# Kernel optimization log

Measured on AMD Instinct MI355X. Metric: run time of the kernel, lower is better.

## Reference

```python
import jax, jax.numpy as jnp
import numpy as np

B, N, CS, CV, K = 8, 2048, 256, 128, 3
EPS = 1e-6


def _eq_layernorm(s, v):
    # scalars: standard layernorm over channels; vectors: RMS of channel norms (equivariant)
    mu = s.mean(-1, keepdims=True)
    var = ((s - mu) ** 2).mean(-1, keepdims=True)
    s = (s - mu) * jax.lax.rsqrt(var + EPS)
    n2 = (v ** 2).sum(-1).mean(-1, keepdims=True)  # [b,n,1]
    v = v * jax.lax.rsqrt(n2 + EPS)[..., None]
    return s, v


def setup_inputs() -> dict:
    key = jax.random.key(0)
    ks = jax.random.split(key, 7)
    fan_s = K * (CS + CV)       # 1152
    fan_v = K * (CS + 2 * CV)   # 1536
    return {
        "x_s": jax.random.normal(ks[0], (B, N, CS), jnp.float32),
        "x_v": jax.random.normal(ks[1], (B, N, CV, 3), jnp.float32),
        "coords": jax.random.normal(ks[2], (B, N, 3), jnp.float32) * 10.0,
        "W_conv_s": jax.random.normal(ks[3], (fan_s, CS), jnp.float32),
        "W_conv_v": jax.random.normal(ks[4], (fan_v, CV), jnp.float32),
        "W_si_s": jax.random.normal(ks[5], (CS, CS), jnp.float32),
        "W_si_v": jax.random.normal(ks[6], (CV, CV), jnp.float32),
    }


def reference(x_s, x_v, coords, W_conv_s, W_conv_v, W_si_s, W_si_v):
    b, n, cs = x_s.shape
    cv = x_v.shape[2]
    pad = K // 2
    # 'same' padding: zeros for features, edge for coords (zero displacement at boundary)
    sp = jnp.pad(x_s, ((0, 0), (pad, pad), (0, 0)))
    vp = jnp.pad(x_v, ((0, 0), (pad, pad), (0, 0), (0, 0)))
    cp = jnp.pad(coords, ((0, 0), (pad, pad), (0, 0)), mode="edge")
    s_win = jnp.stack([sp[:, k:k + n] for k in range(K)], 2)   # [b,n,K,cs]
    v_win = jnp.stack([vp[:, k:k + n] for k in range(K)], 2)   # [b,n,K,cv,3]
    c_win = jnp.stack([cp[:, k:k + n] for k in range(K)], 2)   # [b,n,K,3]

    d = c_win - coords[:, :, None, :]
    dn = jnp.linalg.norm(d, axis=-1, keepdims=True)
    rhat = d * jnp.where(dn > 1e-6, 1.0 / jnp.maximum(dn, 1e-6), 0.0)

    # Clebsch-Gordan paths of (0e,1e) features with sh = (1, rhat)
    vdot = jnp.einsum("bnkcd,bnkd->bnkc", v_win, rhat)                    # 1x1 -> 0
    scal_in = jnp.concatenate([s_win, vdot], -1).reshape(b, n, -1)        # [b,n,K*(cs+cv)]
    s_rhat = s_win[..., None] * rhat[:, :, :, None, :]                    # 0x1 -> 1
    v_cross = jnp.cross(v_win, rhat[:, :, :, None, :])                    # 1x1 -> 1
    vec_in = jnp.concatenate([v_win, s_rhat, v_cross], 3).reshape(b, n, -1, 3)

    # SequenceConvolution linear mixing (fan-in normalized) + norm=True
    h_s = jnp.einsum("bnp,po->bno", scal_in, W_conv_s) / float(np.sqrt(scal_in.shape[-1]))
    h_v = jnp.einsum("bnpd,po->bnod", vec_in, W_conv_v) / float(np.sqrt(vec_in.shape[2]))
    h_s, h_v = _eq_layernorm(h_s, h_v)

    # SelfInteraction: per-degree channel mixing, residual=True, norm_last=True
    y_s = h_s + h_s @ W_si_s / float(np.sqrt(cs))
    y_v = h_v + jnp.einsum("bncd,co->bnod", h_v, W_si_v) / float(np.sqrt(cv))
    y_s, y_v = _eq_layernorm(y_s, y_v)

    # block Residual + final EquivariantLayerNorm
    z_s, z_v = _eq_layernorm(x_s + y_s, x_v + y_v)
    return z_s, z_v
```

## Files before the change

kernel.cpp:

```cpp
#include <hip/hip_runtime.h>
#include <hip/hip_bf16.h>


typedef __attribute__((ext_vector_type(8))) short short8;
typedef __attribute__((ext_vector_type(4))) float f32x4;
typedef unsigned short u16;

#define B_   8
#define N_   2048
#define EPS_ 1e-6f
#define TB   64

#define OFF_CS 0
#define OFF_V  294912
#define OFF_G  393216
#define OFF_SS 491520
#define OFF_SV 557056

#define MFMA(a,b,c) __builtin_amdgcn_mfma_f32_16x16x32_bf16((a),(b),(c),0,0,0)

__device__ __forceinline__ u16 f2b(float v){ __hip_bfloat16 h=__float2bfloat16(v); return *(u16*)&h; }

__global__ __launch_bounds__(256) void prep_weights(
    const float* __restrict__ Wcs, const float* __restrict__ Wcv,
    const float* __restrict__ Wss, const float* __restrict__ Wsv,
    u16* __restrict__ ws)
{
    const int bid = blockIdx.x;
    const float* src; int N, r0, ld, c0; u16* dst; int tile;
    if (bid < 288)      { src=Wcs; N=256; r0=0; dst=ws+OFF_CS; ld=1152; c0=0; tile=bid; }
    else if (bid < 336) { int k=(bid-288)/16; tile=(bid-288)%16;
                          src=Wcv; N=128; r0=k*512;     dst=ws+OFF_V; ld=768; c0=k*256; }
    else if (bid < 432) { int k=(bid-336)/32; tile=(bid-336)%32;
                          src=Wcv; N=128; r0=k*512+128; dst=ws+OFF_G; ld=768; c0=k*256; }
    else if (bid < 480) { int k=(bid-432)/16; tile=(bid-432)%16;
                          src=Wcv; N=128; r0=k*512+384; dst=ws+OFF_V; ld=768; c0=k*256+128; }
    else if (bid < 544) { tile=bid-480; src=Wss; N=256; r0=0; dst=ws+OFF_SS; ld=256; c0=0; }
    else                { tile=bid-544; src=Wsv; N=128; r0=0; dst=ws+OFF_SV; ld=128; c0=0; }
    const int ntN = N >> 5;
    const int kt = (tile/ntN)*32, nn = (tile%ntN)*32;
    __shared__ float t[32][33];
    const int r = threadIdx.x >> 5, c = threadIdx.x & 31;
#pragma unroll
    for (int i = 0; i < 4; ++i)
        t[r+8*i][c] = src[(size_t)(r0+kt+r+8*i)*N + nn+c];
    __syncthreads();
#pragma unroll
    for (int i = 0; i < 4; ++i)
        dst[(size_t)(nn+r+8*i)*ld + c0+kt+c] = f2b(t[c][r+8*i]);
}

__device__ __forceinline__ void ln_reduce(
    float p1[4][4], float p2[4][4], float pv[4][4], f32x4* red,
    int tid, int lm, int lq4, int w,
    float mu[4][4], float ss[4][4], float vs[4][4])
{
    __syncthreads();
#pragma unroll
    for (int m2 = 1; m2 < 16; m2 <<= 1)
#pragma unroll
        for (int m = 0; m < 4; ++m)
#pragma unroll
            for (int q = 0; q < 4; ++q) {
                p1[m][q] += __shfl_xor(p1[m][q], m2);
                p2[m][q] += __shfl_xor(p2[m][q], m2);
                pv[m][q] += __shfl_xor(pv[m][q], m2);
            }
    if (lm == 0)
#pragma unroll
        for (int m = 0; m < 4; ++m)
#pragma unroll
            for (int q = 0; q < 4; ++q) {
                f32x4 r = {p1[m][q], p2[m][q], pv[m][q], 0.f};
                red[(m*16+lq4+q)*8 + w] = r;
            }
    __syncthreads();
    if (tid < 64) {
        const int t = tid;
        f32x4 rs = red[t*8+0];
#pragma unroll
        for (int i = 1; i < 8; ++i) rs += red[t*8+i];
        const float mm = rs.x * (1.f/256.f);
        f32x4 fin;
        fin.x = mm;
        fin.y = rsqrtf(rs.y*(1.f/256.f) - mm*mm + EPS_);
        fin.z = rsqrtf(rs.z*(1.f/128.f) + EPS_);
        fin.w = 0.f;
        red[t*8 + (t&7)] = fin;
    }
    __syncthreads();
#pragma unroll
    for (int m = 0; m < 4; ++m)
#pragma unroll
        for (int q = 0; q < 4; ++q) {
            const int t = m*16 + lq4 + q;
            const f32x4 fin = red[t*8 + (t&7)];
            mu[m][q] = fin.x; ss[m][q] = fin.y; vs[m][q] = fin.z;
        }
}

__global__ __launch_bounds__(512, 2) void mixing_main(
    const float* __restrict__ x_s, const float* __restrict__ x_v,
    const float* __restrict__ coords, const u16* __restrict__ wt,
    float* __restrict__ out)
{
    __shared__ __align__(16) char smem[162816];
    u16*   fs  = (u16*)smem;
    u16*   fv  = (u16*)(smem + 50176);
    u16*   hsb = (u16*)smem;
    u16*   hvb = (u16*)(smem + 50176);
    float* xvL = (float*)(smem + 50176);
    float* rhp = (float*)(smem + 151552);
    f32x4* red = (f32x4*)(smem + 154624);

    const int tid = threadIdx.x;
    const int w   = tid >> 6, l = tid & 63;
    const int lm  = l & 15, lk8 = (l >> 4) << 3, lq4 = (l >> 4) << 2;
    const int wh2 = w & 3;
    const int th  = w >> 2;
    const int gt0 = blockIdx.x * TB;
    const int n0  = gt0 & (N_ - 1);
    const int seq0 = gt0 - n0;
    const size_t ZV0 = (size_t)B_ * N_ * 256;

    if (tid < 192) {
        const int t = tid / 3, k = tid - 3 * (tid / 3);
        const int jn = n0 + t + k - 1;
        const int jc = jn < 0 ? 0 : (jn > N_-1 ? N_-1 : jn);
        const float* cj = coords + (size_t)(seq0 + jc) * 3;
        const float* c0p = coords + (size_t)(gt0 + t) * 3;
        const float d0 = cj[0]-c0p[0], d1 = cj[1]-c0p[1], d2 = cj[2]-c0p[2];
        const float dn = sqrtf(d0*d0 + d1*d1 + d2*d2);
        const float inv = dn > 1e-6f ? 1.f/dn : 0.f;
        rhp[(t*3+k)*4+0] = d0*inv; rhp[(t*3+k)*4+1] = d1*inv; rhp[(t*3+k)*4+2] = d2*inv;
    }
    __syncthreads();

    const f32x4 fz = {0.f,0.f,0.f,0.f};
    f32x4 acc_s[4][2];
    f32x4 accv[3][2][2];
#pragma unroll
    for (int m = 0; m < 4; ++m) { acc_s[m][0] = fz; acc_s[m][1] = fz; }
#pragma unroll
    for (int d = 0; d < 3; ++d)
#pragma unroll
        for (int tf = 0; tf < 2; ++tf) { accv[d][tf][0] = fz; accv[d][tf][1] = fz; }

    const int bt = tid >> 3;
    const int bx = tid & 7;

#pragma unroll 1
    for (int k = 0; k < 3; ++k) {
        const int jn = n0 + bt + k - 1;
        const bool valid = (unsigned)jn < (unsigned)N_;
        const size_t j = (size_t)seq0 + (valid ? jn : 0);
        {
            const int c0 = bx * 32;
            const float4* sp = (const float4*)(x_s + j*256 + c0);
#pragma unroll
            for (int h = 0; h < 4; ++h) {
                float v[8];
                if (valid) {
                    const float4 f0 = sp[2*h], f1 = sp[2*h+1];
                    v[0]=f0.x; v[1]=f0.y; v[2]=f0.z; v[3]=f0.w;
                    v[4]=f1.x; v[5]=f1.y; v[6]=f1.z; v[7]=f1.w;
                } else {
#pragma unroll
                    for (int i = 0; i < 8; ++i) v[i] = 0.f;
                }
                short8 p;
#pragma unroll
                for (int i = 0; i < 8; ++i) p[i] = (short)f2b(v[i]);
                *(short8*)(fs + bt*392 + c0 + 8*h) = p;
            }
        }
        {
            const int ch0 = bx * 16;
            const float r0 = rhp[(bt*3+k)*4+0];
            const float r1 = rhp[(bt*3+k)*4+1];
            const float r2 = rhp[(bt*3+k)*4+2];
#pragma unroll
            for (int hh = 0; hh < 2; ++hh) {
                const int cb = ch0 + 8*hh;
                float vv[24];
                if (valid) {
                    const float4* vp = (const float4*)(x_v + ((size_t)j*128 + cb)*3);
#pragma unroll
                    for (int i = 0; i < 6; ++i) {
                        const float4 f = vp[i];
                        vv[4*i]=f.x; vv[4*i+1]=f.y; vv[4*i+2]=f.z; vv[4*i+3]=f.w;
                    }
                } else {
#pragma unroll
                    for (int i = 0; i < 24; ++i) vv[i] = 0.f;
                }
                short8 dv, w0, w1, w2, x0, x1, x2;
#pragma unroll
                for (int m = 0; m < 8; ++m) {
                    const float a0 = vv[3*m], a1 = vv[3*m+1], a2 = vv[3*m+2];
                    dv[m] = (short)f2b(a0*r0 + a1*r1 + a2*r2);
                    w0[m] = (short)f2b(a0); w1[m] = (short)f2b(a1); w2[m] = (short)f2b(a2);
                    x0[m] = (short)f2b(a1*r2 - a2*r1);
                    x1[m] = (short)f2b(a2*r0 - a0*r2);
                    x2[m] = (short)f2b(a0*r1 - a1*r0);
                }
                *(short8*)(fs + bt*392 + 256 + cb)            = dv;
                *(short8*)(fv + (0*64+bt)*264 + cb)           = w0;
                *(short8*)(fv + (1*64+bt)*264 + cb)           = w1;
                *(short8*)(fv + (2*64+bt)*264 + cb)           = w2;
                *(short8*)(fv + (0*64+bt)*264 + 128 + cb)     = x0;
                *(short8*)(fv + (1*64+bt)*264 + 128 + cb)     = x1;
                *(short8*)(fv + (2*64+bt)*264 + 128 + cb)     = x2;
            }
        }

        const u16* bS0 = wt + OFF_CS + k*384 + (size_t)((2*w+0)*16+lm)*1152;
        const u16* bS1 = wt + OFF_CS + k*384 + (size_t)((2*w+1)*16+lm)*1152;
        const u16* bG0 = wt + OFF_G  + k*256 + (size_t)((2*wh2+0)*16+lm)*768;
        const u16* bG1 = wt + OFF_G  + k*256 + (size_t)((2*wh2+1)*16+lm)*768;
        const u16* bV0 = wt + OFF_V  + k*256 + (size_t)((2*wh2+0)*16+lm)*768;
        const u16* bV1 = wt + OFF_V  + k*256 + (size_t)((2*wh2+1)*16+lm)*768;
        short8 Bs0[3], Bs1[3];
#pragma unroll
        for (int i = 0; i < 3; ++i) {
            Bs0[i] = *(const short8*)(bS0 + i*32 + lk8);
            Bs1[i] = *(const short8*)(bS1 + i*32 + lk8);
        }
        short8 pg0 = *(const short8*)(bG0 + lk8);
        short8 pg1 = *(const short8*)(bG1 + lk8);
        short8 pv0 = *(const short8*)(bV0 + lk8);
        short8 pv1 = *(const short8*)(bV1 + lk8);
        __syncthreads();

        f32x4 agc[2][2] = {{fz,fz},{fz,fz}};
#pragma unroll
        for (int ks = 0; ks < 12; ++ks) {
            const int r = ks % 3;
            const short8 b0 = Bs0[r], b1 = Bs1[r];
            if (ks + 3 < 12) {
                Bs0[r] = *(const short8*)(bS0 + (ks+3)*32 + lk8);
                Bs1[r] = *(const short8*)(bS1 + (ks+3)*32 + lk8);
            }
            const int ko = ks*32 + lk8;
            const short8 a0 = *(const short8*)(fs + ( 0+lm)*392 + ko);
            const short8 a1 = *(const short8*)(fs + (16+lm)*392 + ko);
            const short8 a2 = *(const short8*)(fs + (32+lm)*392 + ko);
            const short8 a3 = *(const short8*)(fs + (48+lm)*392 + ko);
            acc_s[0][0] = MFMA(a0, b0, acc_s[0][0]);
            acc_s[0][1] = MFMA(a0, b1, acc_s[0][1]);
            acc_s[1][0] = MFMA(a1, b0, acc_s[1][0]);
            acc_s[1][1] = MFMA(a1, b1, acc_s[1][1]);
            acc_s[2][0] = MFMA(a2, b0, acc_s[2][0]);
            acc_s[2][1] = MFMA(a2, b1, acc_s[2][1]);
            acc_s[3][0] = MFMA(a3, b0, acc_s[3][0]);
            acc_s[3][1] = MFMA(a3, b1, acc_s[3][1]);
            if (ks < 8) {
                const short8 g0 = pg0, g1 = pg1;
                if (ks < 7) {
                    pg0 = *(const short8*)(bG0 + (ks+1)*32 + lk8);
                    pg1 = *(const short8*)(bG1 + (ks+1)*32 + lk8);
                }
                if (th == 0) {
                    agc[0][0] = MFMA(a0, g0, agc[0][0]);
                    agc[0][1] = MFMA(a0, g1, agc[0][1]);
                    agc[1][0] = MFMA(a1, g0, agc[1][0]);
                    agc[1][1] = MFMA(a1, g1, agc[1][1]);
                } else {
                    agc[0][0] = MFMA(a2, g0, agc[0][0]);
                    agc[0][1] = MFMA(a2, g1, agc[0][1]);
                    agc[1][0] = MFMA(a3, g0, agc[1][0]);
                    agc[1][1] = MFMA(a3, g1, agc[1][1]);
                }
            }
        }
#pragma unroll
        for (int ks = 0; ks < 8; ++ks) {
            const int ko = ks*32 + lk8;
            const short8 bv0 = pv0, bv1 = pv1;
            if (ks < 7) {
                pv0 = *(const short8*)(bV0 + (ks+1)*32 + lk8);
                pv1 = *(const short8*)(bV1 + (ks+1)*32 + lk8);
            }
#pragma unroll
            for (int d = 0; d < 3; ++d)
#pragma unroll
                for (int tf = 0; tf < 2; ++tf) {
                    const short8 a = *(const short8*)(
                        fv + (d*64 + (2*th+tf)*16 + lm)*264 + ko);
                    accv[d][tf][0] = MFMA(a, bv0, accv[d][tf][0]);
                    accv[d][tf][1] = MFMA(a, bv1, accv[d][tf][1]);
                }
        }
#pragma unroll
        for (int d = 0; d < 3; ++d)
#pragma unroll
            for (int tf = 0; tf < 2; ++tf)
#pragma unroll
                for (int u2 = 0; u2 < 2; ++u2)
#pragma unroll
                    for (int q = 0; q < 4; ++q) {
                        const int t = (2*th+tf)*16 + lq4 + q;
                        accv[d][tf][u2][q] += agc[tf][u2][q] * rhp[(t*3+k)*4+d];
                    }
        __syncthreads();
    }

    const float inv_fs = 0.029462783f;
    const float inv_fv = 0.0255155136f;
#pragma unroll
    for (int m = 0; m < 4; ++m)
#pragma unroll
        for (int u = 0; u < 2; ++u)
#pragma unroll
            for (int q = 0; q < 4; ++q) acc_s[m][u][q] *= inv_fs;
#pragma unroll
    for (int d = 0; d < 3; ++d)
#pragma unroll
        for (int tf = 0; tf < 2; ++tf)
#pragma unroll
            for (int u2 = 0; u2 < 2; ++u2)
#pragma unroll
                for (int q = 0; q < 4; ++q) accv[d][tf][u2][q] *= inv_fv;

    float p1[4][4], p2[4][4], pv[4][4], mu[4][4], ss[4][4], vs[4][4];
    float vstA[4], vstB[4];
#pragma unroll
    for (int q = 0; q < 4; ++q) {
        float cA = 0.f, cB = 0.f;
#pragma unroll
        for (int d = 0; d < 3; ++d)
#pragma unroll
            for (int u2 = 0; u2 < 2; ++u2) {
                const float xa = accv[d][0][u2][q]; cA += xa*xa;
                const float xb = accv[d][1][u2][q]; cB += xb*xb;
            }
#pragma unroll
        for (int m = 0; m < 4; ++m) {
            float a = 0.f, b = 0.f;
#pragma unroll
            for (int u = 0; u < 2; ++u) { const float x = acc_s[m][u][q]; a += x; b += x*x; }
            p1[m][q] = a; p2[m][q] = b;
            pv[m][q] = (m == 2*th) ? cA : ((m == 2*th+1) ? cB : 0.f);
        }
    }
    ln_reduce(p1, p2, pv, red, tid, lm, lq4, w, mu, ss, vs);
#pragma unroll
    for (int q = 0; q < 4; ++q) {
        vstA[q] = th ? vs[2][q] : vs[0][q];
        vstB[q] = th ? vs[3][q] : vs[1][q];
    }

#pragma unroll
    for (int m = 0; m < 4; ++m)
#pragma unroll
        for (int u = 0; u < 2; ++u)
#pragma unroll
            for (int q = 0; q < 4; ++q) {
                const float h = (acc_s[m][u][q] - mu[m][q]) * ss[m][q];
                acc_s[m][u][q] = h;
                hsb[(m*16+lq4+q)*264 + (2*w+u)*16 + lm] = f2b(h);
            }
#pragma unroll
    for (int d = 0; d < 3; ++d)
#pragma unroll
        for (int tf = 0; tf < 2; ++tf)
#pragma unroll
            for (int u2 = 0; u2 < 2; ++u2)
#pragma unroll
                for (int q = 0; q < 4; ++q) {
                    const float h = accv[d][tf][u2][q] * (tf ? vstB[q] : vstA[q]);
                    accv[d][tf][u2][q] = h;
                    hvb[(d*64 + (2*th+tf)*16 + lq4 + q)*136 + (2*wh2+u2)*16 + lm] = f2b(h);
                }

    const u16* bP0 = wt + OFF_SS + (size_t)((2*w+0)*16+lm)*256;
    const u16* bP1 = wt + OFF_SS + (size_t)((2*w+1)*16+lm)*256;
    const u16* cQ0 = wt + OFF_SV + (size_t)((2*wh2+0)*16+lm)*128;
    const u16* cQ1 = wt + OFF_SV + (size_t)((2*wh2+1)*16+lm)*128;
    short8 Cs0[3], Cs1[3];
#pragma unroll
    for (int i = 0; i < 3; ++i) {
        Cs0[i] = *(const short8*)(bP0 + i*32 + lk8);
        Cs1[i] = *(const short8*)(bP1 + i*32 + lk8);
    }
    short8 pq0 = *(const short8*)(cQ0 + lk8);
    short8 pq1 = *(const short8*)(cQ1 + lk8);
    __syncthreads();

    f32x4 accs[4][2];
    f32x4 accw[3][2][2];
#pragma unroll
    for (int m = 0; m < 4; ++m) { accs[m][0] = fz; accs[m][1] = fz; }
#pragma unroll
    for (int d = 0; d < 3; ++d)
#pragma unroll
        for (int tf = 0; tf < 2; ++tf) { accw[d][tf][0] = fz; accw[d][tf][1] = fz; }
#pragma unroll
    for (int ks = 0; ks < 8; ++ks) {
        const int r = ks % 3;
        const short8 c0 = Cs0[r], c1 = Cs1[r];
        if (ks + 3 < 8) {
            Cs0[r] = *(const short8*)(bP0 + (ks+3)*32 + lk8);
            Cs1[r] = *(const short8*)(bP1 + (ks+3)*32 + lk8);
        }
        const int ko = ks*32 + lk8;
#pragma unroll
        for (int m = 0; m < 4; ++m) {
            const short8 a = *(const short8*)(hsb + (m*16+lm)*264 + ko);
            accs[m][0] = MFMA(a, c0, accs[m][0]);
            accs[m][1] = MFMA(a, c1, accs[m][1]);
        }
    }
#pragma unroll
    for (int ks = 0; ks < 4; ++ks) {
        const int ko = ks*32 + lk8;
        const short8 c0 = pq0, c1 = pq1;
        if (ks < 3) {
            pq0 = *(const short8*)(cQ0 + (ks+1)*32 + lk8);
            pq1 = *(const short8*)(cQ1 + (ks+1)*32 + lk8);
        }
#pragma unroll
        for (int d = 0; d < 3; ++d)
#pragma unroll
            for (int tf = 0; tf < 2; ++tf) {
                const short8 a = *(const short8*)(
                    hvb + (d*64 + (2*th+tf)*16 + lm)*136 + ko);
                accw[d][tf][0] = MFMA(a, c0, accw[d][tf][0]);
                accw[d][tf][1] = MFMA(a, c1, accw[d][tf][1]);
            }
    }

#pragma unroll
    for (int m = 0; m < 4; ++m)
#pragma unroll
        for (int u = 0; u < 2; ++u)
#pragma unroll
            for (int q = 0; q < 4; ++q) acc_s[m][u][q] += accs[m][u][q] * 0.0625f;
#pragma unroll
    for (int d = 0; d < 3; ++d)
#pragma unroll
        for (int tf = 0; tf < 2; ++tf)
#pragma unroll
            for (int u2 = 0; u2 < 2; ++u2)
#pragma unroll
                for (int q = 0; q < 4; ++q)
                    accv[d][tf][u2][q] += accw[d][tf][u2][q] * 0.08838834764f;

#pragma unroll
    for (int q = 0; q < 4; ++q) {
        float cA = 0.f, cB = 0.f;
#pragma unroll
        for (int d = 0; d < 3; ++d)
#pragma unroll
            for (int u2 = 0; u2 < 2; ++u2) {
                const float xa = accv[d][0][u2][q]; cA += xa*xa;
                const float xb = accv[d][1][u2][q]; cB += xb*xb;
            }
#pragma unroll
        for (int m = 0; m < 4; ++m) {
            float a = 0.f, b = 0.f;
#pragma unroll
            for (int u = 0; u < 2; ++u) { const float x = acc_s[m][u][q]; a += x; b += x*x; }
            p1[m][q] = a; p2[m][q] = b;
            pv[m][q] = (m == 2*th) ? cA : ((m == 2*th+1) ? cB : 0.f);
        }
    }
    float4 xr[12];
    {
        const float4* xvsrc = (const float4*)(x_v + (size_t)gt0 * 384);
#pragma unroll
        for (int i = 0; i < 12; ++i) xr[i] = xvsrc[tid + i*512];
    }
    ln_reduce(p1, p2, pv, red, tid, lm, lq4, w, mu, ss, vs);
#pragma unroll
    for (int q = 0; q < 4; ++q) {
        vstA[q] = th ? vs[2][q] : vs[0][q];
        vstB[q] = th ? vs[3][q] : vs[1][q];
    }
#pragma unroll
    for (int i = 0; i < 12; ++i) {
        const int e4 = tid + i*512;
        const int t = e4 / 96, c4 = e4 - t*96;
        *(float4*)(xvL + t*388 + c4*4) = xr[i];
    }
    __syncthreads();

#pragma unroll
    for (int m = 0; m < 4; ++m)
#pragma unroll
        for (int u = 0; u < 2; ++u)
#pragma unroll
            for (int q = 0; q < 4; ++q)
                acc_s[m][u][q] = (acc_s[m][u][q] - mu[m][q]) * ss[m][q]
                    + x_s[(size_t)(gt0 + m*16 + lq4 + q)*256 + (2*w+u)*16 + lm];
#pragma unroll
    for (int d = 0; d < 3; ++d)
#pragma unroll
        for (int tf = 0; tf < 2; ++tf)
#pragma unroll
            for (int u2 = 0; u2 < 2; ++u2)
#pragma unroll
                for (int q = 0; q < 4; ++q) {
                    const int t = (2*th+tf)*16 + lq4 + q;
                    accv[d][tf][u2][q] = accv[d][tf][u2][q] * (tf ? vstB[q] : vstA[q])
                        + xvL[t*388 + ((2*wh2+u2)*16 + lm)*3 + d];
                }

#pragma unroll
    for (int q = 0; q < 4; ++q) {
        float cA = 0.f, cB = 0.f;
#pragma unroll
        for (int d = 0; d < 3; ++d)
#pragma unroll
            for (int u2 = 0; u2 < 2; ++u2) {
                const float xa = accv[d][0][u2][q]; cA += xa*xa;
                const float xb = accv[d][1][u2][q]; cB += xb*xb;
            }
#pragma unroll
        for (int m = 0; m < 4; ++m) {
            float a = 0.f, b = 0.f;
#pragma unroll
            for (int u = 0; u < 2; ++u) { const float x = acc_s[m][u][q]; a += x; b += x*x; }
            p1[m][q] = a; p2[m][q] = b;
            pv[m][q] = (m == 2*th) ? cA : ((m == 2*th+1) ? cB : 0.f);
        }
    }
    ln_reduce(p1, p2, pv, red, tid, lm, lq4, w, mu, ss, vs);
#pragma unroll
    for (int q = 0; q < 4; ++q) {
        vstA[q] = th ? vs[2][q] : vs[0][q];
        vstB[q] = th ? vs[3][q] : vs[1][q];
    }

#pragma unroll
    for (int m = 0; m < 4; ++m)
#pragma unroll
        for (int u = 0; u < 2; ++u)
#pragma unroll
            for (int q = 0; q < 4; ++q)
                out[(size_t)(gt0 + m*16 + lq4 + q)*256 + (2*w+u)*16 + lm] =
                    (acc_s[m][u][q] - mu[m][q]) * ss[m][q];
#pragma unroll
    for (int d = 0; d < 3; ++d)
#pragma unroll
        for (int tf = 0; tf < 2; ++tf)
#pragma unroll
            for (int u2 = 0; u2 < 2; ++u2)
#pragma unroll
                for (int q = 0; q < 4; ++q) {
                    const int t = (2*th+tf)*16 + lq4 + q;
                    xvL[t*388 + ((2*wh2+u2)*16 + lm)*3 + d] =
                        accv[d][tf][u2][q] * (tf ? vstB[q] : vstA[q]);
                }
    __syncthreads();
    {
        f32x4* dst = (f32x4*)(out + ZV0 + (size_t)gt0 * 384);
#pragma unroll
        for (int i = 0; i < 12; ++i) {
            const int e4 = tid + i*512;
            const int t = e4 / 96, c4 = e4 - t*96;
            const f32x4 v = *(const f32x4*)(xvL + t*388 + c4*4);
            __builtin_nontemporal_store(v, dst + e4);
        }
    }
}

extern "C" void kernel_launch(void* const* d_in, const int* in_sizes, int n_in,
                              void* d_out, int out_size, void* d_ws, size_t ws_size,
                              hipStream_t stream) {
    const float* x_s    = (const float*)d_in[0];
    const float* x_v    = (const float*)d_in[1];
    const float* coords = (const float*)d_in[2];
    const float* Wcs    = (const float*)d_in[3];
    const float* Wcv    = (const float*)d_in[4];
    const float* Wss    = (const float*)d_in[5];
    const float* Wsv    = (const float*)d_in[6];
    float* out = (float*)d_out;
    u16* ws = (u16*)d_ws;

    hipLaunchKernelGGL(prep_weights, dim3(560), dim3(256), 0, stream,
                       Wcs, Wcv, Wss, Wsv, ws);
    hipLaunchKernelGGL(mixing_main, dim3((B_ * N_) / TB), dim3(512), 0, stream,
                       x_s, x_v, coords, ws, out);
}
```

Measured before the change: 105.4 us.

## Split block into scalar and vector warp groups with 1024 threads

Doubles the block to 1024 threads and gives each half of the warps one job: group 0 computes the scalar path and group 1 computes the gate and vector path. This replaces the old scheme where every warp interleaved scalar, gate and vector MFMAs, shortening each warp's serial chain and splitting register pressure between the groups. The LayerNorm reduction is rewritten to match, with group-specific partial sums written to a swizzled shared buffer. In exchange, occupancy drops to one 1024-thread block per CU with a tighter per-thread register budget, and the two groups may have uneven amounts of work.

```diff
diff --git a/kernel.cpp b/kernel.cpp
--- a/kernel.cpp
+++ b/kernel.cpp
@@ -3,6 +3,7 @@
 
 
 typedef __attribute__((ext_vector_type(8))) short short8;
+typedef __attribute__((ext_vector_type(4))) short short4v;
 typedef __attribute__((ext_vector_type(4))) float f32x4;
 typedef unsigned short u16;
 
@@ -50,56 +51,116 @@
         dst[(size_t)(nn+r+8*i)*ld + c0+kt+c] = f2b(t[c][r+8*i]);
 }
 
-__device__ __forceinline__ void ln_reduce(
-    float p1[4][4], float p2[4][4], float pv[4][4], f32x4* red,
-    int tid, int lm, int lq4, int w,
-    float mu[4][4], float ss[4][4], float vs[4][4])
+#define PSLOT(t, i) ((t)*32 + ((((i)+(t)) & 7) << 2))
+
+__device__ __forceinline__ void ln_pass(
+    const f32x4 acc_s[4][2], const f32x4 accv[3][2][2],
+    float* redf, int tid, int lm, int lq4, int grp, int sw, int th,
+    float mu[4][4], float ss[4][4], float vstA[4], float vstB[4])
 {
     __syncthreads();
-#pragma unroll
-    for (int m2 = 1; m2 < 16; m2 <<= 1)
+    if (grp == 0) {
+        float p1[4][4], p2[4][4];
 #pragma unroll
         for (int m = 0; m < 4; ++m)
 #pragma unroll
             for (int q = 0; q < 4; ++q) {
-                p1[m][q] += __shfl_xor(p1[m][q], m2);
-                p2[m][q] += __shfl_xor(p2[m][q], m2);
-                pv[m][q] += __shfl_xor(pv[m][q], m2);
-            }
-    if (lm == 0)
-#pragma unroll
-        for (int m = 0; m < 4; ++m)
+                float a = 0.f, b = 0.f;
+#pragma unroll
+                for (int u = 0; u < 2; ++u) { const float x = acc_s[m][u][q]; a += x; b += x*x; }
+                p1[m][q] = a; p2[m][q] = b;
+            }
+#pragma unroll
+        for (int m2 = 1; m2 < 16; m2 <<= 1)
+#pragma unroll
+            for (int m = 0; m < 4; ++m)
+#pragma unroll
+                for (int q = 0; q < 4; ++q) {
+                    p1[m][q] += __shfl_xor(p1[m][q], m2);
+                    p2[m][q] += __shfl_xor(p2[m][q], m2);
+                }
+        if (lm == 0)
+#pragma unroll
+            for (int m = 0; m < 4; ++m)
+#pragma unroll
+                for (int q = 0; q < 4; ++q) {
+                    const int t = m*16 + lq4 + q;
+                    redf[PSLOT(t, sw) + 0] = p1[m][q];
+                    redf[PSLOT(t, sw) + 1] = p2[m][q];
+                }
+    } else {
+        float cA[4], cB[4];
+#pragma unroll
+        for (int q = 0; q < 4; ++q) {
+            float a = 0.f, b = 0.f;
+#pragma unroll
+            for (int d = 0; d < 3; ++d)
+#pragma unroll
+                for (int u2 = 0; u2 < 2; ++u2) {
+                    const float xa = accv[d][0][u2][q]; a += xa*xa;
+                    const float xb = accv[d][1][u2][q]; b += xb*xb;
+                }
+            cA[q] = a; cB[q] = b;
+        }
+#pragma unroll
+        for (int m2 = 1; m2 < 16; m2 <<= 1)
 #pragma unroll
             for (int q = 0; q < 4; ++q) {
-                f32x4 r = {p1[m][q], p2[m][q], pv[m][q], 0.f};
-                red[(m*16+lq4+q)*8 + w] = r;
-            }
+                cA[q] += __shfl_xor(cA[q], m2);
+                cB[q] += __shfl_xor(cB[q], m2);
+            }
+        if (lm == 0)
+#pragma unroll
+            for (int q = 0; q < 4; ++q) {
+                const int tA = (2*th+0)*16 + lq4 + q;
+                const int tB = (2*th+1)*16 + lq4 + q;
+                redf[PSLOT(tA, sw) + 2] = cA[q];
+                redf[PSLOT(tB, sw) + 2] = cB[q];
+            }
+    }
     __syncthreads();
     if (tid < 64) {
         const int t = tid;
-        f32x4 rs = red[t*8+0];
-#pragma unroll
-        for (int i = 1; i < 8; ++i) rs += red[t*8+i];
-        const float mm = rs.x * (1.f/256.f);
+        float s1 = 0.f, s2 = 0.f, sv = 0.f;
+#pragma unroll
+        for (int i = 0; i < 8; ++i) {
+            s1 += redf[PSLOT(t, i) + 0];
+            s2 += redf[PSLOT(t, i) + 1];
+        }
+        const int base = (t >= 32) ? 4 : 0;
+#pragma unroll
+        for (int i = 0; i < 4; ++i)
+            sv += redf[PSLOT(t, base + i) + 2];
+        const float mm = s1 * (1.f/256.f);
         f32x4 fin;
         fin.x = mm;
-        fin.y = rsqrtf(rs.y*(1.f/256.f) - mm*mm + EPS_);
-        fin.z = rsqrtf(rs.z*(1.f/128.f) + EPS_);
+        fin.y = rsqrtf(s2*(1.f/256.f) - mm*mm + EPS_);
+        fin.z = rsqrtf(sv*(1.f/128.f) + EPS_);
         fin.w = 0.f;
-        red[t*8 + (t&7)] = fin;
-    }
-    __syncthreads();
-#pragma unroll
-    for (int m = 0; m < 4; ++m)
+        *(f32x4*)(redf + PSLOT(t, t & 7)) = fin;
+    }
+    __syncthreads();
+    if (grp == 0) {
+#pragma unroll
+        for (int m = 0; m < 4; ++m)
+#pragma unroll
+            for (int q = 0; q < 4; ++q) {
+                const int t = m*16 + lq4 + q;
+                const f32x4 fin = *(const f32x4*)(redf + PSLOT(t, t & 7));
+                mu[m][q] = fin.x; ss[m][q] = fin.y;
+            }
+    } else {
 #pragma unroll
         for (int q = 0; q < 4; ++q) {
-            const int t = m*16 + lq4 + q;
-            const f32x4 fin = red[t*8 + (t&7)];
-            mu[m][q] = fin.x; ss[m][q] = fin.y; vs[m][q] = fin.z;
-        }
+            const int tA = (2*th+0)*16 + lq4 + q;
+            const int tB = (2*th+1)*16 + lq4 + q;
+            vstA[q] = redf[PSLOT(tA, tA & 7) + 2];
+            vstB[q] = redf[PSLOT(tB, tB & 7) + 2];
+        }
+    }
 }
 
-__global__ __launch_bounds__(512, 2) void mixing_main(
+__global__ __launch_bounds__(1024) void mixing_main(
     const float* __restrict__ x_s, const float* __restrict__ x_v,
     const float* __restrict__ coords, const u16* __restrict__ wt,
     float* __restrict__ out)
@@ -111,13 +172,15 @@
     u16*   hvb = (u16*)(smem + 50176);
     float* xvL = (float*)(smem + 50176);
     float* rhp = (float*)(smem + 151552);
-    f32x4* red = (f32x4*)(smem + 154624);
+    float* redf = (float*)(smem + 154624);
 
     const int tid = threadIdx.x;
     const int w   = tid >> 6, l = tid & 63;
     const int lm  = l & 15, lk8 = (l >> 4) << 3, lq4 = (l >> 4) << 2;
-    const int wh2 = w & 3;
-    const int th  = w >> 2;
+    const int grp = w >> 3;
+    const int sw  = w & 7;
+    const int th  = sw >> 2;
+    const int wh2 = sw & 3;
     const int gt0 = blockIdx.x * TB;
     const int n0  = gt0 & (N_ - 1);
     const int seq0 = gt0 - n0;
@@ -139,15 +202,18 @@
     const f32x4 fz = {0.f,0.f,0.f,0.f};
     f32x4 acc_s[4][2];
     f32x4 accv[3][2][2];
-#pragma unroll
-    for (int m = 0; m < 4; ++m) { acc_s[m][0] = fz; acc_s[m][1] = fz; }
-#pragma unroll
-    for (int d = 0; d < 3; ++d)
-#pragma unroll
-        for (int tf = 0; tf < 2; ++tf) { accv[d][tf][0] = fz; accv[d][tf][1] = fz; }
-
-    const int bt = tid >> 3;
-    const int bx = tid & 7;
+    if (grp == 0) {
+#pragma unroll
+        for (int m = 0; m < 4; ++m) { acc_s[m][0] = fz; acc_s[m][1] = fz; }
+    } else {
+#pragma unroll
+        for (int d = 0; d < 3; ++d)
+#pragma unroll
+            for (int tf = 0; tf < 2; ++tf) { accv[d][tf][0] = fz; accv[d][tf][1] = fz; }
+    }
+
+    const int bt = tid >> 4;
+    const int bx = tid & 15;
 
 #pragma unroll 1
     for (int k = 0; k < 3; ++k) {
@@ -155,48 +221,47 @@
         const bool valid = (unsigned)jn < (unsigned)N_;
         const size_t j = (size_t)seq0 + (valid ? jn : 0);
         {
-            const int c0 = bx * 32;
-            const float4* sp = (const float4*)(x_s + j*256 + c0);
-#pragma unroll
-            for (int h = 0; h < 4; ++h) {
-                float v[8];
-                if (valid) {
-                    const float4 f0 = sp[2*h], f1 = sp[2*h+1];
-                    v[0]=f0.x; v[1]=f0.y; v[2]=f0.z; v[3]=f0.w;
-                    v[4]=f1.x; v[5]=f1.y; v[6]=f1.z; v[7]=f1.w;
-                } else {
-#pragma unroll
-                    for (int i = 0; i < 8; ++i) v[i] = 0.f;
-                }
-                short8 p;
-#pragma unroll
-                for (int i = 0; i < 8; ++i) p[i] = (short)f2b(v[i]);
-                *(short8*)(fs + bt*392 + c0 + 8*h) = p;
-            }
+            const int c0 = bx * 16;
+            float v[16];
+            if (valid) {
+                const float4* sp = (const float4*)(x_s + j*256 + c0);
+#pragma unroll
+                for (int i = 0; i < 4; ++i) {
+                    const float4 f = sp[i];
+                    v[4*i]=f.x; v[4*i+1]=f.y; v[4*i+2]=f.z; v[4*i+3]=f.w;
+                }
+            } else {
+#pragma unroll
+                for (int i = 0; i < 16; ++i) v[i] = 0.f;
+            }
+            short8 p0, p1;
+#pragma unroll
+            for (int i = 0; i < 8; ++i) { p0[i]=(short)f2b(v[i]); p1[i]=(short)f2b(v[8+i]); }
+            *(short8*)(fs + bt*392 + c0)     = p0;
+            *(short8*)(fs + bt*392 + c0 + 8) = p1;
         }
         {
-            const int ch0 = bx * 16;
+            const int c0 = bx * 8;
             const float r0 = rhp[(bt*3+k)*4+0];
             const float r1 = rhp[(bt*3+k)*4+1];
             const float r2 = rhp[(bt*3+k)*4+2];
 #pragma unroll
             for (int hh = 0; hh < 2; ++hh) {
-                const int cb = ch0 + 8*hh;
-                float vv[24];
+                float vv[12];
                 if (valid) {
-                    const float4* vp = (const float4*)(x_v + ((size_t)j*128 + cb)*3);
-#pragma unroll
-                    for (int i = 0; i < 6; ++i) {
+                    const float4* vp = (const float4*)(x_v + ((size_t)j*128 + c0 + 4*hh)*3);
+#pragma unroll
+                    for (int i = 0; i < 3; ++i) {
                         const float4 f = vp[i];
                         vv[4*i]=f.x; vv[4*i+1]=f.y; vv[4*i+2]=f.z; vv[4*i+3]=f.w;
                     }
                 } else {
 #pragma unroll
-                    for (int i = 0; i < 24; ++i) vv[i] = 0.f;
-                }
-                short8 dv, w0, w1, w2, x0, x1, x2;
-#pragma unroll
-                for (int m = 0; m < 8; ++m) {
+                    for (int i = 0; i < 12; ++i) vv[i] = 0.f;
+                }
+                short4v dv, w0, w1, w2, x0, x1, x2;
+#pragma unroll
+                for (int m = 0; m < 4; ++m) {
                     const float a0 = vv[3*m], a1 = vv[3*m+1], a2 = vv[3*m+2];
                     dv[m] = (short)f2b(a0*r0 + a1*r1 + a2*r2);
                     w0[m] = (short)f2b(a0); w1[m] = (short)f2b(a1); w2[m] = (short)f2b(a2);
@@ -204,93 +269,247 @@
                     x1[m] = (short)f2b(a2*r0 - a0*r2);
                     x2[m] = (short)f2b(a0*r1 - a1*r0);
                 }
-                *(short8*)(fs + bt*392 + 256 + cb)            = dv;
-                *(short8*)(fv + (0*64+bt)*264 + cb)           = w0;
-                *(short8*)(fv + (1*64+bt)*264 + cb)           = w1;
-                *(short8*)(fv + (2*64+bt)*264 + cb)           = w2;
-                *(short8*)(fv + (0*64+bt)*264 + 128 + cb)     = x0;
-                *(short8*)(fv + (1*64+bt)*264 + 128 + cb)     = x1;
-                *(short8*)(fv + (2*64+bt)*264 + 128 + cb)     = x2;
-            }
-        }
-
-        const u16* bS0 = wt + OFF_CS + k*384 + (size_t)((2*w+0)*16+lm)*1152;
-        const u16* bS1 = wt + OFF_CS + k*384 + (size_t)((2*w+1)*16+lm)*1152;
+                const int cc = c0 + 4*hh;
+                *(short4v*)(fs + bt*392 + 256 + cc)          = dv;
+                *(short4v*)(fv + (0*64+bt)*264 + cc)         = w0;
+                *(short4v*)(fv + (1*64+bt)*264 + cc)         = w1;
+                *(short4v*)(fv + (2*64+bt)*264 + cc)         = w2;
+                *(short4v*)(fv + (0*64+bt)*264 + 128 + cc)   = x0;
+                *(short4v*)(fv + (1*64+bt)*264 + 128 + cc)   = x1;
+                *(short4v*)(fv + (2*64+bt)*264 + 128 + cc)   = x2;
+            }
+        }
+
+        const u16* bS0 = wt + OFF_CS + k*384 + (size_t)((2*sw+0)*16+lm)*1152;
+        const u16* bS1 = wt + OFF_CS + k*384 + (size_t)((2*sw+1)*16+lm)*1152;
         const u16* bG0 = wt + OFF_G  + k*256 + (size_t)((2*wh2+0)*16+lm)*768;
         const u16* bG1 = wt + OFF_G  + k*256 + (size_t)((2*wh2+1)*16+lm)*768;
         const u16* bV0 = wt + OFF_V  + k*256 + (size_t)((2*wh2+0)*16+lm)*768;
         const u16* bV1 = wt + OFF_V  + k*256 + (size_t)((2*wh2+1)*16+lm)*768;
-        short8 Bs0[3], Bs1[3];
-#pragma unroll
-        for (int i = 0; i < 3; ++i) {
-            Bs0[i] = *(const short8*)(bS0 + i*32 + lk8);
-            Bs1[i] = *(const short8*)(bS1 + i*32 + lk8);
-        }
-        short8 pg0 = *(const short8*)(bG0 + lk8);
-        short8 pg1 = *(const short8*)(bG1 + lk8);
-        short8 pv0 = *(const short8*)(bV0 + lk8);
-        short8 pv1 = *(const short8*)(bV1 + lk8);
+        short8 pb0, pb1, pg0, pg1, pv0, pv1;
+        if (grp == 0) {
+            pb0 = *(const short8*)(bS0 + lk8);
+            pb1 = *(const short8*)(bS1 + lk8);
+        } else {
+            pg0 = *(const short8*)(bG0 + lk8);
+            pg1 = *(const short8*)(bG1 + lk8);
+            pv0 = *(const short8*)(bV0 + lk8);
+            pv1 = *(const short8*)(bV1 + lk8);
+        }
         __syncthreads();
 
-        f32x4 agc[2][2] = {{fz,fz},{fz,fz}};
-#pragma unroll
-        for (int ks = 0; ks < 12; ++ks) {
-            const int r = ks % 3;
-            const short8 b0 = Bs0[r], b1 = Bs1[r];
-            if (ks + 3 < 12) {
-                Bs0[r] = *(const short8*)(bS0 + (ks+3)*32 + lk8);
-                Bs1[r] = *(const short8*)(bS1 + (ks+3)*32 + lk8);
-            }
-            const int ko = ks*32 + lk8;
-            const short8 a0 = *(const short8*)(fs + ( 0+lm)*392 + ko);
-            const short8 a1 = *(const short8*)(fs + (16+lm)*392 + ko);
-            const short8 a2 = *(const short8*)(fs + (32+lm)*392 + ko);
-            const short8 a3 = *(const short8*)(fs + (48+lm)*392 + ko);
-            acc_s[0][0] = MFMA(a0, b0, acc_s[0][0]);
-            acc_s[0][1] = MFMA(a0, b1, acc_s[0][1]);
-            acc_s[1][0] = MFMA(a1, b0, acc_s[1][0]);
-            acc_s[1][1] = MFMA(a1, b1, acc_s[1][1]);
-            acc_s[2][0] = MFMA(a2, b0, acc_s[2][0]);
-            acc_s[2][1] = MFMA(a2, b1, acc_s[2][1]);
-            acc_s[3][0] = MFMA(a3, b0, acc_s[3][0]);
-            acc_s[3][1] = MFMA(a3, b1, acc_s[3][1]);
-            if (ks < 8) {
-                const short8 g0 = pg0, g1 = pg1;
+        if (grp == 0) {
+#pragma unroll
+            for (int ks = 0; ks < 12; ++ks) {
+                const short8 b0 = pb0, b1 = pb1;
+                if (ks < 11) {
+                    pb0 = *(const short8*)(bS0 + (ks+1)*32 + lk8);
+                    pb1 = *(const short8*)(bS1 + (ks+1)*32 + lk8);
+                }
+                const int ko = ks*32 + lk8;
+                const short8 a0 = *(const short8*)(fs + ( 0+lm)*392 + ko);
+                const short8 a1 = *(const short8*)(fs + (16+lm)*392 + ko);
+                const short8 a2 = *(const short8*)(fs + (32+lm)*392 + ko);
+                const short8 a3 = *(const short8*)(fs + (48+lm)*392 + ko);
+                acc_s[0][0] = MFMA(a0, b0, acc_s[0][0]);
+                acc_s[0][1] = MFMA(a0, b1, acc_s[0][1]);
+                acc_s[1][0] = MFMA(a1, b0, acc_s[1][0]);
+                acc_s[1][1] = MFMA(a1, b1, acc_s[1][1]);
+                acc_s[2][0] = MFMA(a2, b0, acc_s[2][0]);
+                acc_s[2][1] = MFMA(a2, b1, acc_s[2][1]);
+                acc_s[3][0] = MFMA(a3, b0, acc_s[3][0]);
+                acc_s[3][1] = MFMA(a3, b1, acc_s[3][1]);
+            }
+        } else {
+            f32x4 agc[2][2] = {{fz,fz},{fz,fz}};
+#pragma unroll
+            for (int ks = 0; ks < 8; ++ks) {
+                const short8 g0 = pg0, g1 = pg1, bv0 = pv0, bv1 = pv1;
                 if (ks < 7) {
                     pg0 = *(const short8*)(bG0 + (ks+1)*32 + lk8);
                     pg1 = *(const short8*)(bG1 + (ks+1)*32 + lk8);
-                }
-                if (th == 0) {
-                    agc[0][0] = MFMA(a0, g0, agc[0][0]);
-                    agc[0][1] = MFMA(a0, g1, agc[0][1]);
-                    agc[1][0] = MFMA(a1, g0, agc[1][0]);
-                    agc[1][1] = MFMA(a1, g1, agc[1][1]);
-                } else {
-                    agc[0][0] = MFMA(a2, g0, agc[0][0]);
-                    agc[0][1] = MFMA(a2, g1, agc[0][1]);
-                    agc[1][0] = MFMA(a3, g0, agc[1][0]);
-                    agc[1][1] = MFMA(a3, g1, agc[1][1]);
-                }
-            }
-        }
+                    pv0 = *(const short8*)(bV0 + (ks+1)*32 + lk8);
+                    pv1 = *(const short8*)(bV1 + (ks+1)*32 + lk8);
+                }
+                const int ko = ks*32 + lk8;
+                const short8 ag0 = *(const short8*)(fs + ((2*th+0)*16+lm)*392 + ko);
+                const short8 ag1 = *(const short8*)(fs + ((2*th+1)*16+lm)*392 + ko);
+                agc[0][0] = MFMA(ag0, g0, agc[0][0]);
+                agc[0][1] = MFMA(ag0, g1, agc[0][1]);
+                agc[1][0] = MFMA(ag1, g0, agc[1][0]);
+                agc[1][1] = MFMA(ag1, g1, agc[1][1]);
+#pragma unroll
+                for (int d = 0; d < 3; ++d)
+#pragma unroll
+                    for (int tf = 0; tf < 2; ++tf) {
+                        const short8 a = *(const short8*)(
+                            fv + (d*64 + (2*th+tf)*16 + lm)*264 + ko);
+                        accv[d][tf][0] = MFMA(a, bv0, accv[d][tf][0]);
+                        accv[d][tf][1] = MFMA(a, bv1, accv[d][tf][1]);
+                    }
+            }
+#pragma unroll
+            for (int d = 0; d < 3; ++d)
+#pragma unroll
+                for (int tf = 0; tf < 2; ++tf)
+#pragma unroll
+                    for (int u2 = 0; u2 < 2; ++u2)
+#pragma unroll
+                        for (int q = 0; q < 4; ++q) {
+                            const int t = (2*th+tf)*16 + lq4 + q;
+                            accv[d][tf][u2][q] += agc[tf][u2][q] * rhp[(t*3+k)*4+d];
+                        }
+        }
+        __syncthreads();
+    }
+
+    if (grp == 0) {
+#pragma unroll
+        for (int m = 0; m < 4; ++m)
+#pragma unroll
+            for (int u = 0; u < 2; ++u)
+#pragma unroll
+                for (int q = 0; q < 4; ++q) acc_s[m][u][q] *= 0.029462783f;
+    } else {
+#pragma unroll
+        for (int d = 0; d < 3; ++d)
+#pragma unroll
+            for (int tf = 0; tf < 2; ++tf)
+#pragma unroll
+                for (int u2 = 0; u2 < 2; ++u2)
+#pragma unroll
+                    for (int q = 0; q < 4; ++q) accv[d][tf][u2][q] *= 0.0255155136f;
+    }
+
+    float mu[4][4], ss[4][4], vstA[4], vstB[4];
+
+    ln_pass(acc_s, accv, redf, tid, lm, lq4, grp, sw, th, mu, ss, vstA, vstB);
+
+    if (grp == 0) {
+#pragma unroll
+        for (int m = 0; m < 4; ++m)
+#pragma unroll
+            for (int u = 0; u < 2; ++u)
+#pragma unroll
+                for (int q = 0; q < 4; ++q) {
+                    const float h = (acc_s[m][u][q] - mu[m][q]) * ss[m][q];
+                    acc_s[m][u][q] = h;
+                    hsb[(m*16+lq4+q)*264 + (2*sw+u)*16 + lm] = f2b(h);
+                }
+    } else {
+#pragma unroll
+        for (int d = 0; d < 3; ++d)
+#pragma unroll
+            for (int tf = 0; tf < 2; ++tf)
+#pragma unroll
+                for (int u2 = 0; u2 < 2; ++u2)
+#pragma unroll
+                    for (int q = 0; q < 4; ++q) {
+                        const float h = accv[d][tf][u2][q] * (tf ? vstB[q] : vstA[q]);
+                        accv[d][tf][u2][q] = h;
+                        hvb[(d*64 + (2*th+tf)*16 + lq4 + q)*136 + (2*wh2+u2)*16 + lm] = f2b(h);
+                    }
+    }
+
+    const u16* bP0 = wt + OFF_SS + (size_t)((2*sw+0)*16+lm)*256;
+    const u16* bP1 = wt + OFF_SS + (size_t)((2*sw+1)*16+lm)*256;
+    const u16* cQ0 = wt + OFF_SV + (size_t)((2*wh2+0)*16+lm)*128;
+    const u16* cQ1 = wt + OFF_SV + (size_t)((2*wh2+1)*16+lm)*128;
+    short8 pc0, pc1, pq0, pq1;
+    if (grp == 0) {
+        pc0 = *(const short8*)(bP0 + lk8);
+        pc1 = *(const short8*)(bP1 + lk8);
+    } else {
+        pq0 = *(const short8*)(cQ0 + lk8);
+        pq1 = *(const short8*)(cQ1 + lk8);
+    }
+    __syncthreads();
+
+    if (grp == 0) {
+        f32x4 accs[4][2];
+#pragma unroll
+        for (int m = 0; m < 4; ++m) { accs[m][0] = fz; accs[m][1] = fz; }
 #pragma unroll
         for (int ks = 0; ks < 8; ++ks) {
+            const short8 c0 = pc0, c1 = pc1;
+            if (ks < 7) {
+                pc0 = *(const short8*)(bP0 + (ks+1)*32 + lk8);
+                pc1 = *(const short8*)(bP1 + (ks+1)*32 + lk8);
+            }
             const int ko = ks*32 + lk8;
-            const short8 bv0 = pv0, bv1 = pv1;
-            if (ks < 7) {
-                pv0 = *(const short8*)(bV0 + (ks+1)*32 + lk8);
-                pv1 = *(const short8*)(bV1 + (ks+1)*32 + lk8);
-            }
+#pragma unroll
+            for (int m = 0; m < 4; ++m) {
+                const short8 a = *(const short8*)(hsb + (m*16+lm)*264 + ko);
+                accs[m][0] = MFMA(a, c0, accs[m][0]);
+                accs[m][1] = MFMA(a, c1, accs[m][1]);
+            }
+        }
+#pragma unroll
+        for (int m = 0; m < 4; ++m)
+#pragma unroll
+            for (int u = 0; u < 2; ++u)
+#pragma unroll
+                for (int q = 0; q < 4; ++q) acc_s[m][u][q] += accs[m][u][q] * 0.0625f;
+    } else {
+        f32x4 accw[3][2][2];
+#pragma unroll
+        for (int d = 0; d < 3; ++d)
+#pragma unroll
+            for (int tf = 0; tf < 2; ++tf) { accw[d][tf][0] = fz; accw[d][tf][1] = fz; }
+#pragma unroll
+        for (int ks = 0; ks < 4; ++ks) {
+            const short8 c0 = pq0, c1 = pq1;
+            if (ks < 3) {
+                pq0 = *(const short8*)(cQ0 + (ks+1)*32 + lk8);
+                pq1 = *(const short8*)(cQ1 + (ks+1)*32 + lk8);
+            }
+            const int ko = ks*32 + lk8;
 #pragma unroll
             for (int d = 0; d < 3; ++d)
 #pragma unroll
                 for (int tf = 0; tf < 2; ++tf) {
                     const short8 a = *(const short8*)(
-                        fv + (d*64 + (2*th+tf)*16 + lm)*264 + ko);
-                    accv[d][tf][0] = MFMA(a, bv0, accv[d][tf][0]);
-                    accv[d][tf][1] = MFMA(a, bv1, accv[d][tf][1]);
-                }
-        }
+                        hvb + (d*64 + (2*th+tf)*16 + lm)*136 + ko);
+                    accw[d][tf][0] = MFMA(a, c0, accw[d][tf][0]);
+                    accw[d][tf][1] = MFMA(a, c1, accw[d][tf][1]);
+                }
+        }
+#pragma unroll
+        for (int d = 0; d < 3; ++d)
+#pragma unroll
+            for (int tf = 0; tf < 2; ++tf)
+#pragma unroll
+                for (int u2 = 0; u2 < 2; ++u2)
+#pragma unroll
+                    for (int q = 0; q < 4; ++q)
+                        accv[d][tf][u2][q] += accw[d][tf][u2][q] * 0.08838834764f;
+    }
+
+    float4 xr[6];
+    {
+        const float4* xvsrc = (const float4*)(x_v + (size_t)gt0 * 384);
+#pragma unroll
+        for (int i = 0; i < 6; ++i) xr[i] = xvsrc[tid + i*1024];
+    }
+    ln_pass(acc_s, accv, redf, tid, lm, lq4, grp, sw, th, mu, ss, vstA, vstB);
+#pragma unroll
+    for (int i = 0; i < 6; ++i) {
+        const int e4 = tid + i*1024;
+        const int t = e4 / 96, c4 = e4 - t*96;
+        *(float4*)(xvL + t*388 + c4*4) = xr[i];
+    }
+    __syncthreads();
+
+    if (grp == 0) {
+#pragma unroll
+        for (int m = 0; m < 4; ++m)
+#pragma unroll
+            for (int u = 0; u < 2; ++u)
+#pragma unroll
+                for (int q = 0; q < 4; ++q)
+                    acc_s[m][u][q] = (acc_s[m][u][q] - mu[m][q]) * ss[m][q]
+                        + x_s[(size_t)(gt0 + m*16 + lq4 + q)*256 + (2*sw+u)*16 + lm];
+    } else {
 #pragma unroll
         for (int d = 0; d < 3; ++d)
 #pragma unroll
@@ -300,264 +519,42 @@
 #pragma unroll
                     for (int q = 0; q < 4; ++q) {
                         const int t = (2*th+tf)*16 + lq4 + q;
-                        accv[d][tf][u2][q] += agc[tf][u2][q] * rhp[(t*3+k)*4+d];
+                        accv[d][tf][u2][q] = accv[d][tf][u2][q] * (tf ? vstB[q] : vstA[q])
+                            + xvL[t*388 + ((2*wh2+u2)*16 + lm)*3 + d];
                     }
-        __syncthreads();
-    }
-
-    const float inv_fs = 0.029462783f;
-    const float inv_fv = 0.0255155136f;
-#pragma unroll
-    for (int m = 0; m < 4; ++m)
-#pragma unroll
-        for (int u = 0; u < 2; ++u)
-#pragma unroll
-            for (int q = 0; q < 4; ++q) acc_s[m][u][q] *= inv_fs;
-#pragma unroll
-    for (int d = 0; d < 3; ++d)
-#pragma unroll
-        for (int tf = 0; tf < 2; ++tf)
-#pragma unroll
-            for (int u2 = 0; u2 < 2; ++u2)
-#pragma unroll
-                for (int q = 0; q < 4; ++q) accv[d][tf][u2][q] *= inv_fv;
-
-    float p1[4][4], p2[4][4], pv[4][4], mu[4][4], ss[4][4], vs[4][4];
-    float vstA[4], vstB[4];
-#pragma unroll
-    for (int q = 0; q < 4; ++q) {
-        float cA = 0.f, cB = 0.f;
-#pragma unroll
-        for (int d = 0; d < 3; ++d)
-#pragma unroll
-            for (int u2 = 0; u2 < 2; ++u2) {
-                const float xa = accv[d][0][u2][q]; cA += xa*xa;
-                const float xb = accv[d][1][u2][q]; cB += xb*xb;
-            }
-#pragma unroll
-        for (int m = 0; m < 4; ++m) {
-            float a = 0.f, b = 0.f;
-#pragma unroll
-            for (int u = 0; u < 2; ++u) { const float x = acc_s[m][u][q]; a += x; b += x*x; }
-            p1[m][q] = a; p2[m][q] = b;
-            pv[m][q] = (m == 2*th) ? cA : ((m == 2*th+1) ? cB : 0.f);
-        }
-    }
-    ln_reduce(p1, p2, pv, red, tid, lm, lq4, w, mu, ss, vs);
-#pragma unroll
-    for (int q = 0; q < 4; ++q) {
-        vstA[q] = th ? vs[2][q] : vs[0][q];
-        vstB[q] = th ? vs[3][q] : vs[1][q];
-    }
-
-#pragma unroll
-    for (int m = 0; m < 4; ++m)
-#pragma unroll
-        for (int u = 0; u < 2; ++u)
-#pragma unroll
-            for (int q = 0; q < 4; ++q) {
-                const float h = (acc_s[m][u][q] - mu[m][q]) * ss[m][q];
-                acc_s[m][u][q] = h;
-                hsb[(m*16+lq4+q)*264 + (2*w+u)*16 + lm] = f2b(h);
-            }
-#pragma unroll
-    for (int d = 0; d < 3; ++d)
-#pragma unroll
-        for (int tf = 0; tf < 2; ++tf)
-#pragma unroll
-            for (int u2 = 0; u2 < 2; ++u2)
-#pragma unroll
-                for (int q = 0; q < 4; ++q) {
-                    const float h = accv[d][tf][u2][q] * (tf ? vstB[q] : vstA[q]);
-                    accv[d][tf][u2][q] = h;
-                    hvb[(d*64 + (2*th+tf)*16 + lq4 + q)*136 + (2*wh2+u2)*16 + lm] = f2b(h);
-                }
-
-    const u16* bP0 = wt + OFF_SS + (size_t)((2*w+0)*16+lm)*256;
-    const u16* bP1 = wt + OFF_SS + (size_t)((2*w+1)*16+lm)*256;
-    const u16* cQ0 = wt + OFF_SV + (size_t)((2*wh2+0)*16+lm)*128;
-    const u16* cQ1 = wt + OFF_SV + (size_t)((2*wh2+1)*16+lm)*128;
-    short8 Cs0[3], Cs1[3];
-#pragma unroll
-    for (int i = 0; i < 3; ++i) {
-        Cs0[i] = *(const short8*)(bP0 + i*32 + lk8);
-        Cs1[i] = *(const short8*)(bP1 + i*32 + lk8);
-    }
-    short8 pq0 = *(const short8*)(cQ0 + lk8);
-    short8 pq1 = *(const short8*)(cQ1 + lk8);
-    __syncthreads();
-
-    f32x4 accs[4][2];
-    f32x4 accw[3][2][2];
-#pragma unroll
-    for (int m = 0; m < 4; ++m) { accs[m][0] = fz; accs[m][1] = fz; }
-#pragma unroll
-    for (int d = 0; d < 3; ++d)
-#pragma unroll
-        for (int tf = 0; tf < 2; ++tf) { accw[d][tf][0] = fz; accw[d][tf][1] = fz; }
-#pragma unroll
-    for (int ks = 0; ks < 8; ++ks) {
-        const int r = ks % 3;
-        const short8 c0 = Cs0[r], c1 = Cs1[r];
-        if (ks + 3 < 8) {
-            Cs0[r] = *(const short8*)(bP0 + (ks+3)*32 + lk8);
-            Cs1[r] = *(const short8*)(bP1 + (ks+3)*32 + lk8);
-        }
-        const int ko = ks*32 + lk8;
-#pragma unroll
-        for (int m = 0; m < 4; ++m) {
-            const short8 a = *(const short8*)(hsb + (m*16+lm)*264 + ko);
-            accs[m][0] = MFMA(a, c0, accs[m][0]);
-            accs[m][1] = MFMA(a, c1, accs[m][1]);
-        }
-    }
-#pragma unroll
-    for (int ks = 0; ks < 4; ++ks) {
-        const int ko = ks*32 + lk8;
-        const short8 c0 = pq0, c1 = pq1;
-        if (ks < 3) {
-            pq0 = *(const short8*)(cQ0 + (ks+1)*32 + lk8);
-            pq1 = *(const short8*)(cQ1 + (ks+1)*32 + lk8);
-        }
-#pragma unroll
-        for (int d = 0; d < 3; ++d)
-#pragma unroll
-            for (int tf = 0; tf < 2; ++tf) {
-                const short8 a = *(const short8*)(
-                    hvb + (d*64 + (2*th+tf)*16 + lm)*136 + ko);
-                accw[d][tf][0] = MFMA(a, c0, accw[d][tf][0]);
-                accw[d][tf][1] = MFMA(a, c1, accw[d][tf][1]);
-            }
-    }
-
-#pragma unroll
-    for (int m = 0; m < 4; ++m)
-#pragma unroll
-        for (int u = 0; u < 2; ++u)
-#pragma unroll
-            for (int q = 0; q < 4; ++q) acc_s[m][u][q] += accs[m][u][q] * 0.0625f;
-#pragma unroll
-    for (int d = 0; d < 3; ++d)
-#pragma unroll
-        for (int tf = 0; tf < 2; ++tf)
-#pragma unroll
-            for (int u2 = 0; u2 < 2; ++u2)
+    }
+
+    ln_pass(acc_s, accv, redf, tid, lm, lq4, grp, sw, th, mu, ss, vstA, vstB);
+
+    if (grp == 0) {
+#pragma unroll
+        for (int m = 0; m < 4; ++m)
+#pragma unroll
+            for (int u = 0; u < 2; ++u)
 #pragma unroll
                 for (int q = 0; q < 4; ++q)
-                    accv[d][tf][u2][q] += accw[d][tf][u2][q] * 0.08838834764f;
-
-#pragma unroll
-    for (int q = 0; q < 4; ++q) {
-        float cA = 0.f, cB = 0.f;
-#pragma unroll
-        for (int d = 0; d < 3; ++d)
-#pragma unroll
-            for (int u2 = 0; u2 < 2; ++u2) {
-                const float xa = accv[d][0][u2][q]; cA += xa*xa;
-                const float xb = accv[d][1][u2][q]; cB += xb*xb;
-            }
-#pragma unroll
-        for (int m = 0; m < 4; ++m) {
-            float a = 0.f, b = 0.f;
-#pragma unroll
-            for (int u = 0; u < 2; ++u) { const float x = acc_s[m][u][q]; a += x; b += x*x; }
-            p1[m][q] = a; p2[m][q] = b;
-            pv[m][q] = (m == 2*th) ? cA : ((m == 2*th+1) ? cB : 0.f);
-        }
-    }
-    float4 xr[12];
-    {
-        const float4* xvsrc = (const float4*)(x_v + (size_t)gt0 * 384);
-#pragma unroll
-        for (int i = 0; i < 12; ++i) xr[i] = xvsrc[tid + i*512];
-    }
-    ln_reduce(p1, p2, pv, red, tid, lm, lq4, w, mu, ss, vs);
-#pragma unroll
-    for (int q = 0; q < 4; ++q) {
-        vstA[q] = th ? vs[2][q] : vs[0][q];
-        vstB[q] = th ? vs[3][q] : vs[1][q];
-    }
-#pragma unroll
-    for (int i = 0; i < 12; ++i) {
-        const int e4 = tid + i*512;
-        const int t = e4 / 96, c4 = e4 - t*96;
-        *(float4*)(xvL + t*388 + c4*4) = xr[i];
-    }
-    __syncthreads();
-
-#pragma unroll
-    for (int m = 0; m < 4; ++m)
-#pragma unroll
-        for (int u = 0; u < 2; ++u)
-#pragma unroll
-            for (int q = 0; q < 4; ++q)
-                acc_s[m][u][q] = (acc_s[m][u][q] - mu[m][q]) * ss[m][q]
-                    + x_s[(size_t)(gt0 + m*16 + lq4 + q)*256 + (2*w+u)*16 + lm];
-#pragma unroll
-    for (int d = 0; d < 3; ++d)
-#pragma unroll
-        for (int tf = 0; tf < 2; ++tf)
-#pragma unroll
-            for (int u2 = 0; u2 < 2; ++u2)
-#pragma unroll
-                for (int q = 0; q < 4; ++q) {
-                    const int t = (2*th+tf)*16 + lq4 + q;
-                    accv[d][tf][u2][q] = accv[d][tf][u2][q] * (tf ? vstB[q] : vstA[q])
-                        + xvL[t*388 + ((2*wh2+u2)*16 + lm)*3 + d];
-                }
-
-#pragma unroll
-    for (int q = 0; q < 4; ++q) {
-        float cA = 0.f, cB = 0.f;
-#pragma unroll
-        for (int d = 0; d < 3; ++d)
-#pragma unroll
-            for (int u2 = 0; u2 < 2; ++u2) {
-                const float xa = accv[d][0][u2][q]; cA += xa*xa;
-                const float xb = accv[d][1][u2][q]; cB += xb*xb;
-            }
-#pragma unroll
-        for (int m = 0; m < 4; ++m) {
-            float a = 0.f, b = 0.f;
-#pragma unroll
-            for (int u = 0; u < 2; ++u) { const float x = acc_s[m][u][q]; a += x; b += x*x; }
-            p1[m][q] = a; p2[m][q] = b;
-            pv[m][q] = (m == 2*th) ? cA : ((m == 2*th+1) ? cB : 0.f);
-        }
-    }
-    ln_reduce(p1, p2, pv, red, tid, lm, lq4, w, mu, ss, vs);
-#pragma unroll
-    for (int q = 0; q < 4; ++q) {
-        vstA[q] = th ? vs[2][q] : vs[0][q];
-        vstB[q] = th ? vs[3][q] : vs[1][q];
-    }
-
-#pragma unroll
-    for (int m = 0; m < 4; ++m)
-#pragma unroll
-        for (int u = 0; u < 2; ++u)
-#pragma unroll
-            for (int q = 0; q < 4; ++q)
-                out[(size_t)(gt0 + m*16 + lq4 + q)*256 + (2*w+u)*16 + lm] =
-                    (acc_s[m][u][q] - mu[m][q]) * ss[m][q];
-#pragma unroll
-    for (int d = 0; d < 3; ++d)
-#pragma unroll
-        for (int tf = 0; tf < 2; ++tf)
-#pragma unroll
-            for (int u2 = 0; u2 < 2; ++u2)
-#pragma unroll
-                for (int q = 0; q < 4; ++q) {
-                    const int t = (2*th+tf)*16 + lq4 + q;
-                    xvL[t*388 + ((2*wh2+u2)*16 + lm)*3 + d] =
-                        accv[d][tf][u2][q] * (tf ? vstB[q] : vstA[q]);
-                }
+                    out[(size_t)(gt0 + m*16 + lq4 + q)*256 + (2*sw+u)*16 + lm] =
+                        (acc_s[m][u][q] - mu[m][q]) * ss[m][q];
+    } else {
+#pragma unroll
+        for (int d = 0; d < 3; ++d)
+#pragma unroll
+            for (int tf = 0; tf < 2; ++tf)
+#pragma unroll
+                for (int u2 = 0; u2 < 2; ++u2)
+#pragma unroll
+                    for (int q = 0; q < 4; ++q) {
+                        const int t = (2*th+tf)*16 + lq4 + q;
+                        xvL[t*388 + ((2*wh2+u2)*16 + lm)*3 + d] =
+                            accv[d][tf][u2][q] * (tf ? vstB[q] : vstA[q]);
+                    }
+    }
     __syncthreads();
     {
         f32x4* dst = (f32x4*)(out + ZV0 + (size_t)gt0 * 384);
 #pragma unroll
-        for (int i = 0; i < 12; ++i) {
-            const int e4 = tid + i*512;
+        for (int i = 0; i < 6; ++i) {
+            const int e4 = tid + i*1024;
             const int t = e4 / 96, c4 = e4 - t*96;
             const f32x4 v = *(const f32x4*)(xvL + t*388 + c4*4);
             __builtin_nontemporal_store(v, dst + e4);
@@ -580,6 +577,6 @@
 
     hipLaunchKernelGGL(prep_weights, dim3(560), dim3(256), 0, stream,
                        Wcs, Wcv, Wss, Wsv, ws);
-    hipLaunchKernelGGL(mixing_main, dim3((B_ * N_) / TB), dim3(512), 0, stream,
+    hipLaunchKernelGGL(mixing_main, dim3((B_ * N_) / TB), dim3(1024), 0, stream,
                        x_s, x_v, coords, ws, out);
 }
```

After: 265.5 us. 2.52x slower.
